# Kernel tuning notes

Hardware: AMD Instinct MI355X
Metric: run time of the kernel (lower is better)

The kernel has to match this reference:

```python
import jax, jax.numpy as jnp
import numpy as np
from jax import lax

STRIDES = (8, 16, 32, 64, 128)
LEVEL_HW = ((100, 128), (50, 64), (25, 32), (13, 16), (7, 8))
N, C = 16, 80
IMG_H, IMG_W = 800, 1024
THRESH = 0.05
IOU_THR = 0.6
PRE_NMS_K = 1000
POST_K = 100
CLS_OFFSET = 4096.0  # > max image coord, separates classes for batched NMS


def setup_inputs() -> dict:
    key = jax.random.key(0)
    ks = jax.random.split(key, 15)
    inp = {}
    for l, (h, w) in enumerate(LEVEL_HW):
        inp[f"cls{l}"] = jax.random.normal(ks[3 * l], (N, C, h, w), dtype=jnp.float32)
        # ltrb distances scaled to realistic pixel extents
        inp[f"reg{l}"] = jax.random.uniform(ks[3 * l + 1], (N, 4, h, w), dtype=jnp.float32) * 128.0
        inp[f"ctr{l}"] = jax.random.normal(ks[3 * l + 2], (N, 1, h, w), dtype=jnp.float32)
    return inp


def _level(cls, reg, ctr, stride):
    n, c, h, w = cls.shape
    sx = jnp.arange(w, dtype=jnp.float32) * stride + stride / 2.0
    sy = jnp.arange(h, dtype=jnp.float32) * stride + stride / 2.0
    px = jnp.broadcast_to(sx[None, :], (h, w)).reshape(-1)  # [hw]
    py = jnp.broadcast_to(sy[:, None], (h, w)).reshape(-1)  # [hw]
    # sqrt(cls_prob * centerness_prob), as in the source
    scores = jnp.sqrt(jax.nn.sigmoid(cls) * jax.nn.sigmoid(ctr))  # [n,c,h,w]
    scores = scores.transpose(0, 2, 3, 1).reshape(n, h * w, c)
    regf = reg.transpose(0, 2, 3, 1).reshape(n, h * w, 4)
    vals = scores.max(axis=-1)          # best class score per location
    labels = scores.argmax(axis=-1)
    vals = jnp.where(vals > THRESH, vals, 0.0)  # score threshold (zeroed instead of dropped)
    x1 = jnp.clip(px[None, :] - regf[..., 0], 0.0, IMG_W)
    y1 = jnp.clip(py[None, :] - regf[..., 1], 0.0, IMG_H)
    x2 = jnp.clip(px[None, :] + regf[..., 2], 0.0, IMG_W)
    y2 = jnp.clip(py[None, :] + regf[..., 3], 0.0, IMG_H)
    boxes = jnp.stack([x1, y1, x2, y2], axis=-1)  # [n,hw,4]
    return vals, labels, boxes


def _pairwise_iou(b):  # b: [K,4]
    area = (b[:, 2] - b[:, 0]) * (b[:, 3] - b[:, 1])
    lt = jnp.maximum(b[:, None, :2], b[None, :, :2])
    rb = jnp.minimum(b[:, None, 2:], b[None, :, 2:])
    wh = jnp.clip(rb - lt, 0.0)
    inter = wh[..., 0] * wh[..., 1]
    return inter / (area[:, None] + area[None, :] - inter + 1e-9)


def _nms_single(boxes, scores, labels):
    # class-aware NMS via per-class coordinate offset (torchvision batched_nms trick)
    ob = boxes + (labels.astype(boxes.dtype) * CLS_OFFSET)[:, None]
    iou = _pairwise_iou(ob)  # [K,K]
    K = boxes.shape[0]
    idxs = jnp.arange(K)

    def body(valid, i):
        keep_i = valid[i]
        valid = valid & ~(keep_i & (iou[i] > IOU_THR) & (idxs > i))
        return valid, keep_i

    _, keeps = lax.scan(body, scores > 0.0, idxs)  # greedy, scores already sorted desc
    kept_scores = jnp.where(keeps, scores, 0.0)
    top_vals, top = lax.top_k(kept_scores, POST_K)
    return boxes[top], top_vals, labels[top]


def _forward(levels):
    vals_l, labels_l, boxes_l = [], [], []
    for cls, reg, ctr, stride in levels:
        v, la, b = _level(cls, reg, ctr, stride)
        vals_l.append(v)
        labels_l.append(la)
        boxes_l.append(b)
    scores = jnp.concatenate(vals_l, axis=1)   # [N,P]
    labels = jnp.concatenate(labels_l, axis=1)  # [N,P]
    boxes = jnp.concatenate(boxes_l, axis=1)    # [N,P,4]
    tv, ti = lax.top_k(scores, PRE_NMS_K)       # pre-NMS top-k, sorted desc
    boxes_k = jnp.take_along_axis(boxes, ti[:, :, None], axis=1)
    labels_k = jnp.take_along_axis(labels, ti, axis=1)
    return jax.vmap(_nms_single)(boxes_k, tv, labels_k)


def reference(cls0, reg0, ctr0, cls1, reg1, ctr1, cls2, reg2, ctr2,
              cls3, reg3, ctr3, cls4, reg4, ctr4):
    levels = [
        (cls0, reg0, ctr0, 8), (cls1, reg1, ctr1, 16), (cls2, reg2, ctr2, 32),
        (cls3, reg3, ctr3, 64), (cls4, reg4, ctr4, 128),
    ]
    boxes, scores, labels = _forward(levels)
    return boxes, scores, labels  # [N,100,4], [N,100], [N,100]
```

## Files before the change

kernel.cpp:

```cpp
#include <hip/hip_runtime.h>
#include <stdint.h>

#pragma clang fp contract(off)

#define NB 16
#define NC 80
#define P_TOT 17064
#define P4 (P_TOT / 4)
#define PRE_K 1000
#define POST_K 100

__device__ __forceinline__ float sigmoidf_(float x) {
  return 1.0f / (1.0f + expf(-x));
}

__global__ __launch_bounds__(256, 2) void decode_kernel(
    const float* __restrict__ cls0, const float* __restrict__ reg0, const float* __restrict__ ctr0,
    const float* __restrict__ cls1, const float* __restrict__ reg1, const float* __restrict__ ctr1,
    const float* __restrict__ cls2, const float* __restrict__ reg2, const float* __restrict__ ctr2,
    const float* __restrict__ cls3, const float* __restrict__ reg3, const float* __restrict__ ctr3,
    const float* __restrict__ cls4, const float* __restrict__ reg4, const float* __restrict__ ctr4,
    int* __restrict__ labels, float* __restrict__ boxes,
    unsigned long long* __restrict__ keys)
{
  int quad = blockIdx.x * 64 + (threadIdx.x >> 2);
  int t4 = threadIdx.x & 3;
  int n = blockIdx.y;
  if (quad >= P4) return;
  int p0 = quad * 4;
  int off, wsh, hw; float stride; const float *cls, *reg, *ctr;
  if (p0 < 12800)      { off = 0;     wsh = 7; hw = 12800; stride = 8.f;   cls = cls0; reg = reg0; ctr = ctr0; }
  else if (p0 < 16000) { off = 12800; wsh = 6; hw = 3200;  stride = 16.f;  cls = cls1; reg = reg1; ctr = ctr1; }
  else if (p0 < 16800) { off = 16000; wsh = 5; hw = 800;   stride = 32.f;  cls = cls2; reg = reg2; ctr = ctr2; }
  else if (p0 < 17008) { off = 16800; wsh = 4; hw = 208;   stride = 64.f;  cls = cls3; reg = reg3; ctr = ctr3; }
  else                 { off = 17008; wsh = 3; hw = 56;    stride = 128.f; cls = cls4; reg = reg4; ctr = ctr4; }
  int loc0 = p0 - off;
  int y = loc0 >> wsh;
  int x0 = loc0 & ((1 << wsh) - 1);
  float py = (float)y * stride + 0.5f * stride;

  int c0 = t4 * 20;
  const float* cptr = cls + (size_t)n * NC * hw + (size_t)c0 * hw + loc0;
  float4 cv[20];
  #pragma unroll
  for (int k = 0; k < 20; ++k)
    cv[k] = *reinterpret_cast<const float4*>(cptr + (size_t)k * hw);

  float best[4] = { -3.4e38f, -3.4e38f, -3.4e38f, -3.4e38f };
  int bl[4] = { c0, c0, c0, c0 };
  #pragma unroll
  for (int k = 0; k < 20; ++k) {
    int c = c0 + k;
    if (cv[k].x > best[0]) { best[0] = cv[k].x; bl[0] = c; }
    if (cv[k].y > best[1]) { best[1] = cv[k].y; bl[1] = c; }
    if (cv[k].z > best[2]) { best[2] = cv[k].z; bl[2] = c; }
    if (cv[k].w > best[3]) { best[3] = cv[k].w; bl[3] = c; }
  }
  #pragma unroll
  for (int e = 0; e < 4; ++e) {
    #pragma unroll
    for (int d = 1; d <= 2; d <<= 1) {
      float ob = __shfl_xor(best[e], d);
      int ol = __shfl_xor(bl[e], d);
      if (ob > best[e] || (ob == best[e] && ol < bl[e])) { best[e] = ob; bl[e] = ol; }
    }
  }

  int e = t4;
  int loce = loc0 + e;
  float sctr_e = sigmoidf_(ctr[(size_t)n * hw + loce]);
  const float* rbase = reg + (size_t)n * 4 * hw + loce;
  float dl = rbase[0];
  float dt = rbase[(size_t)hw];
  float dr = rbase[(size_t)2 * hw];
  float db = rbase[(size_t)3 * hw];

  float s = sqrtf(sigmoidf_(best[e]) * sctr_e);
  float val = (s > 0.05f) ? s : 0.0f;
  float px = (float)(x0 + e) * stride + 0.5f * stride;
  float x1 = fminf(fmaxf(px - dl, 0.f), 1024.f);
  float y1 = fminf(fmaxf(py - dt, 0.f), 800.f);
  float x2 = fminf(fmaxf(px + dr, 0.f), 1024.f);
  float y2 = fminf(fmaxf(py + db, 0.f), 800.f);

  size_t o = (size_t)n * P_TOT + p0 + e;
  labels[o] = bl[e];
  *reinterpret_cast<float4*>(boxes + 4 * o) = make_float4(x1, y1, x2, y2);
  keys[o] = ((unsigned long long)__float_as_uint(val) << 32)
          | (unsigned long long)(0xFFFFFFFFu - (unsigned)(p0 + e));
}

__global__ __launch_bounds__(1024) void topgather_kernel(
    const unsigned long long* __restrict__ keys,
    const float* __restrict__ boxes, const int* __restrict__ labels,
    float* __restrict__ tboxes, float* __restrict__ tscores, int* __restrict__ tlabels)
{
  int n = blockIdx.x;
  int tid = threadIdx.x;
  int wave = tid >> 6;
  int lane = tid & 63;
  __shared__ unsigned hist[16384];
  __shared__ unsigned Wt[16], Wsuf[16];
  __shared__ unsigned s_d, s_M;
  __shared__ unsigned long long skey[2048];

  for (int i = tid; i < 16384; i += 1024) hist[i] = 0;
  __syncthreads();
  const unsigned long long* bk = keys + (size_t)n * P_TOT;
  for (int p = tid; p < P_TOT; p += 1024) {
    unsigned h = (unsigned)(bk[p] >> 48);
    atomicAdd(&hist[h], 1u);
  }
  __syncthreads();

  unsigned bvs[16];
  unsigned ssum = 0;
  #pragma unroll
  for (int q = 0; q < 16; ++q) { bvs[q] = hist[tid * 16 + q]; ssum += bvs[q]; }
  unsigned v = ssum;
  #pragma unroll
  for (int d = 1; d < 64; d <<= 1) {
    unsigned t = __shfl_down(v, d);
    if (lane + d < 64) v += t;
  }
  if (lane == 0) Wt[wave] = v;
  __syncthreads();
  if (wave == 0 && lane < 16) {
    unsigned wv = Wt[lane];
    unsigned own = wv;
    #pragma unroll
    for (int d = 1; d < 16; d <<= 1) {
      unsigned t = __shfl_down(wv, d);
      if (lane + d < 16) wv += t;
    }
    Wsuf[lane] = wv - own;
  }
  __syncthreads();
  unsigned At = v + Wsuf[wave];
  unsigned An = At - ssum;
  {
    if (At >= PRE_K && An < PRE_K) {
      unsigned cum = An;
      int d = tid * 16;
      unsigned M = 0;
      bool done = false;
      #pragma unroll
      for (int b = 15; b >= 0; --b) {
        if (!done) {
          cum += bvs[b];
          if (cum >= PRE_K) { d = tid * 16 + b; M = cum; done = true; }
        }
      }
      s_d = (unsigned)d;
      s_M = M;
    }
  }
  __syncthreads();
  unsigned dsel = s_d;
  {
    unsigned cum = An;
    #pragma unroll
    for (int b = 15; b >= 0; --b) {
      unsigned h = (unsigned)(tid * 16 + b);
      if (h >= dsel) hist[h] = cum << 16;
      cum += bvs[b];
    }
  }
  __syncthreads();
  for (int p = tid; p < P_TOT; p += 1024) {
    unsigned long long k = bk[p];
    unsigned h = (unsigned)(k >> 48);
    if (h >= dsel) {
      unsigned old = atomicAdd(&hist[h], 1u);
      unsigned slot = (old >> 16) + (old & 0xFFFFu);
      if (slot < 2048) skey[slot] = k;
    }
  }
  __syncthreads();
  unsigned Mcap = s_M < 2048u ? s_M : 2048u;
  #pragma unroll
  for (int e = 0; e < 2; ++e) {
    unsigned sidx = (unsigned)tid + e * 1024;
    if (sidx < Mcap) {
      unsigned long long k = skey[sidx];
      unsigned h = (unsigned)(k >> 48);
      unsigned info = hist[h];
      unsigned start = info >> 16;
      unsigned end = start + (info & 0xFFFFu);
      if (end > 2048u) end = 2048u;
      unsigned rank = 0;
      for (unsigned q = start; q < end; ++q)
        rank += (skey[q] > k) ? 1u : 0u;
      unsigned pos = start + rank;
      if (pos < PRE_K) {
        unsigned idx = 0xFFFFFFFFu - (unsigned)(k & 0xFFFFFFFFu);
        float sc = __uint_as_float((unsigned)(k >> 32));
        size_t src = (size_t)n * P_TOT + idx;
        size_t dst = (size_t)n * PRE_K + pos;
        tscores[dst] = sc;
        tlabels[dst] = labels[src];
        *reinterpret_cast<float4*>(tboxes + 4 * dst) =
            *reinterpret_cast<const float4*>(boxes + 4 * src);
      }
    }
  }
}

__global__ __launch_bounds__(128) void iou_kernel(
    const float* __restrict__ tboxes, const int* __restrict__ tlabels,
    unsigned long long* __restrict__ colsupp)
{
  int jb = blockIdx.x, w = blockIdx.y, n = blockIdx.z;
  int tid = threadIdx.x;
  int j = jb * 128 + tid;
  bool jvalid = (j < PRE_K);
  int ibase = w * 64;

  if (ibase >= jb * 128 + 128) {
    if (jvalid) colsupp[((size_t)n * PRE_K + j) * 16 + w] = 0ULL;
    return;
  }

  __shared__ float4 sb[64];
  __shared__ float sa[64];
  if (tid < 64) {
    int i = ibase + tid;
    float4 v = make_float4(0.f, 0.f, 0.f, 0.f);
    if (i < PRE_K) {
      const float* b = tboxes + ((size_t)n * PRE_K + i) * 4;
      float offv = (float)tlabels[(size_t)n * PRE_K + i] * 4096.0f;
      v = make_float4(b[0] + offv, b[1] + offv, b[2] + offv, b[3] + offv);
    }
    sb[tid] = v;
    sa[tid] = (v.z - v.x) * (v.w - v.y);
  }
  __syncthreads();

  float4 bj = make_float4(0.f, 0.f, 0.f, 0.f);
  if (jvalid) {
    const float* b = tboxes + ((size_t)n * PRE_K + j) * 4;
    float offv = (float)tlabels[(size_t)n * PRE_K + j] * 4096.0f;
    bj = make_float4(b[0] + offv, b[1] + offv, b[2] + offv, b[3] + offv);
  }
  float aj = (bj.z - bj.x) * (bj.w - bj.y);

  unsigned long long m = 0, mb = 0;
  #pragma unroll
  for (int b = 0; b < 64; ++b) {
    float4 bi = sb[b];
    float ai = sa[b];
    float lx = fmaxf(bi.x, bj.x), ly = fmaxf(bi.y, bj.y);
    float rx = fminf(bi.z, bj.z), ry = fminf(bi.w, bj.w);
    float iw = fmaxf(rx - lx, 0.f), ih = fmaxf(ry - ly, 0.f);
    float inter = iw * ih;
    float denom = ai + aj - inter + 1e-9f;
    float t = inter - 0.6f * denom;
    if (t > 0.f) m |= (1ull << b);
    if (fabsf(t) <= denom * 7.62939453125e-6f) mb |= (1ull << b);
  }
  if (mb) {
    unsigned long long r = mb;
    while (r) {
      int b = __ffsll(r) - 1; r &= r - 1;
      float4 bi = sb[b];
      float ai = sa[b];
      float lx = fmaxf(bi.x, bj.x), ly = fmaxf(bi.y, bj.y);
      float rx = fminf(bi.z, bj.z), ry = fminf(bi.w, bj.w);
      float iw = fmaxf(rx - lx, 0.f), ih = fmaxf(ry - ly, 0.f);
      float inter = iw * ih;
      float denom = ai + aj - inter + 1e-9f;
      float iou = inter / denom;
      if (iou > 0.6f) m |= (1ull << b); else m &= ~(1ull << b);
    }
  }
  unsigned long long tri;
  if (ibase >= j) tri = 0ULL;
  else if (j - ibase >= 64) tri = ~0ULL;
  else tri = (1ull << (j - ibase)) - 1ull;
  m &= tri;
  if (jvalid) colsupp[((size_t)n * PRE_K + j) * 16 + w] = m;
}

__global__ __launch_bounds__(1024) void greedyfin_kernel(
    const unsigned long long* __restrict__ colsupp, const float* __restrict__ tscores,
    const float* __restrict__ tboxes, const int* __restrict__ tlabels,
    float* __restrict__ out)
{
  int n = blockIdx.x;
  int tid = threadIdx.x;
  int wave = tid >> 6;
  int lane = tid & 63;
  __shared__ unsigned long long T[136 * 64];
  __shared__ unsigned long long keptw[16];

  {
    int wq = wave;
    int j = wq * 64 + lane;
    int base = (wq * (wq + 1)) / 2;
    if (j < PRE_K) {
      const unsigned long long* C = colsupp + ((size_t)n * PRE_K + j) * 16;
      for (int c = 0; c <= wq; ++c) T[(base + c) * 64 + lane] = C[c];
    } else {
      for (int c = 0; c <= wq; ++c) T[(base + c) * 64 + lane] = 0ULL;
    }
  }
  __syncthreads();

  if (wave == 0) {
    const float* sc = tscores + (size_t)n * PRE_K;
    float sval[16];
    #pragma unroll
    for (int k = 0; k < 16; ++k) {
      int j = k * 64 + lane;
      sval[k] = (j < PRE_K) ? sc[j] : 0.f;
    }
    unsigned removedbits = 0;
    #pragma unroll
    for (int c = 0; c < 16; ++c) {
      unsigned long long col = T[((c * (c + 1)) / 2 + c) * 64 + lane];
      unsigned long long sp = __ballot(sval[c] > 0.f);
      unsigned long long inc = __ballot(((removedbits >> c) & 1u) != 0u);
      unsigned long long K = sp & ~inc;
      unsigned long long kept = 0;
      for (int it = 0; it < 64; ++it) {
        unsigned long long Bsupp = __ballot((col & K) != 0ULL);
        unsigned long long Snew = K & ~Bsupp & ~kept;
        if (Snew == 0ULL) break;
        kept |= Snew;
        unsigned long long Bd = __ballot((col & kept) != 0ULL);
        K &= ~Bd;
      }
      if ((col & kept) != 0ULL) removedbits |= (1u << c);
      #pragma unroll
      for (int w = 0; w < 16; ++w) {
        if (w > c) {
          unsigned long long xw = T[((w * (w + 1)) / 2 + c) * 64 + lane];
          if ((xw & kept) != 0ULL) removedbits |= (1u << w);
        }
      }
      if (lane == 0) keptw[c] = kept;
    }
  }
  __syncthreads();

  __shared__ unsigned sk[1024];
  __shared__ unsigned sz[1024];
  bool inr = (tid < PRE_K);
  bool keep = inr && (((keptw[tid >> 6] >> (tid & 63)) & 1ull) != 0ull);
  sk[tid] = keep ? 1u : 0u;
  sz[tid] = (inr && !keep) ? 1u : 0u;
  __syncthreads();
  for (int ofs = 1; ofs < 1024; ofs <<= 1) {
    unsigned a = (tid >= ofs) ? sk[tid - ofs] : 0;
    unsigned b = (tid >= ofs) ? sz[tid - ofs] : 0;
    __syncthreads();
    sk[tid] += a; sz[tid] += b;
    __syncthreads();
  }
  int nk = (int)sk[1023];
  int slot = -1;
  if (inr) {
    if (keep) {
      int r = (int)sk[tid] - 1;
      if (r < POST_K) slot = r;
    } else {
      int r = nk + (int)sz[tid] - 1;
      if (r < POST_K) slot = r;
    }
  }
  if (slot >= 0) {
    size_t src = (size_t)n * PRE_K + tid;
    size_t ob = ((size_t)n * POST_K + slot) * 4;
    out[ob+0] = tboxes[4*src+0];
    out[ob+1] = tboxes[4*src+1];
    out[ob+2] = tboxes[4*src+2];
    out[ob+3] = tboxes[4*src+3];
    out[(size_t)NB*POST_K*4 + (size_t)n*POST_K + slot] = keep ? tscores[src] : 0.0f;
    out[(size_t)NB*POST_K*5 + (size_t)n*POST_K + slot] = (float)tlabels[src];
  }
}

extern "C" void kernel_launch(void* const* d_in, const int* in_sizes, int n_in,
                              void* d_out, int out_size, void* d_ws, size_t ws_size,
                              hipStream_t stream) {
  char* w = (char*)d_ws;
  auto carve = [&](size_t bytes) { char* p = w; w += (bytes + 255) & ~(size_t)255; return p; };
  int* labels   = (int*)carve((size_t)NB * P_TOT * 4);
  float* boxes  = (float*)carve((size_t)NB * P_TOT * 16);
  unsigned long long* keys = (unsigned long long*)carve((size_t)NB * P_TOT * 8);
  unsigned long long* colsupp = (unsigned long long*)carve((size_t)NB * PRE_K * 16 * 8);
  float* tboxes  = (float*)carve((size_t)NB * PRE_K * 16);
  float* tscores = (float*)carve((size_t)NB * PRE_K * 4);
  int* tlabels   = (int*)carve((size_t)NB * PRE_K * 4);

  const float* cls0 = (const float*)d_in[0];
  const float* reg0 = (const float*)d_in[1];
  const float* ctr0 = (const float*)d_in[2];
  const float* cls1 = (const float*)d_in[3];
  const float* reg1 = (const float*)d_in[4];
  const float* ctr1 = (const float*)d_in[5];
  const float* cls2 = (const float*)d_in[6];
  const float* reg2 = (const float*)d_in[7];
  const float* ctr2 = (const float*)d_in[8];
  const float* cls3 = (const float*)d_in[9];
  const float* reg3 = (const float*)d_in[10];
  const float* ctr3 = (const float*)d_in[11];
  const float* cls4 = (const float*)d_in[12];
  const float* reg4 = (const float*)d_in[13];
  const float* ctr4 = (const float*)d_in[14];

  dim3 dg((P4 + 63) / 64, NB);
  decode_kernel<<<dg, 256, 0, stream>>>(cls0, reg0, ctr0, cls1, reg1, ctr1,
                                        cls2, reg2, ctr2, cls3, reg3, ctr3,
                                        cls4, reg4, ctr4,
                                        labels, boxes, keys);
  topgather_kernel<<<NB, 1024, 0, stream>>>(keys, boxes, labels,
                                            tboxes, tscores, tlabels);
  dim3 gi(8, 16, NB);
  iou_kernel<<<gi, 128, 0, stream>>>(tboxes, tlabels, colsupp);
  greedyfin_kernel<<<NB, 1024, 0, stream>>>(colsupp, tscores, tboxes, tlabels, (float*)d_out);
}
```

Measured before the change: 67.42 us.

## Fuse top-k gather, IoU mask, and greedy NMS into one per-image kernel

Merges the top-k selection, pairwise IoU suppression-mask computation and greedy NMS/finalize kernels into a single tail kernel with one block per image. Selected boxes, scores, labels and the triangular mask stay in LDS, aliased over the histogram buffer, so the global round trips and two launches go away. The cost is that IoU work moves from 2048 small blocks spread across the GPU to 16 blocks of 1024 threads, which cuts parallelism and raises LDS use per block.

```diff
diff --git a/kernel.cpp b/kernel.cpp
--- a/kernel.cpp
+++ b/kernel.cpp
@@ -90,22 +90,38 @@
           | (unsigned long long)(0xFFFFFFFFu - (unsigned)(p0 + e));
 }
 
-__global__ __launch_bounds__(1024) void topgather_kernel(
+__global__ __launch_bounds__(1024) void tail_kernel(
     const unsigned long long* __restrict__ keys,
     const float* __restrict__ boxes, const int* __restrict__ labels,
-    float* __restrict__ tboxes, float* __restrict__ tscores, int* __restrict__ tlabels)
+    float* __restrict__ out)
 {
   int n = blockIdx.x;
   int tid = threadIdx.x;
   int wave = tid >> 6;
   int lane = tid & 63;
-  __shared__ unsigned hist[16384];
+
+  __shared__ __align__(16) char smem0[16384 * 4 + 2048 * 8];
+  unsigned* hist = (unsigned*)smem0;
+  unsigned long long* skey = (unsigned long long*)(smem0 + 16384 * 4);
+  unsigned long long* T = (unsigned long long*)smem0;
+  __shared__ float4 tbo[1024];
+  __shared__ float areas[1024];
+  __shared__ float4 tb[1024];
+  __shared__ float sc[1024];
+  __shared__ int lb[1024];
   __shared__ unsigned Wt[16], Wsuf[16];
   __shared__ unsigned s_d, s_M;
-  __shared__ unsigned long long skey[2048];
+  __shared__ unsigned long long keptw[16];
+  __shared__ unsigned sk[1024], sz[1024];
 
   for (int i = tid; i < 16384; i += 1024) hist[i] = 0;
-  __syncthreads();
+  tbo[tid] = make_float4(0.f, 0.f, 0.f, 0.f);
+  areas[tid] = 0.f;
+  tb[tid] = make_float4(0.f, 0.f, 0.f, 0.f);
+  sc[tid] = 0.f;
+  lb[tid] = 0;
+  __syncthreads();
+
   const unsigned long long* bk = keys + (size_t)n * P_TOT;
   for (int p = tid; p < P_TOT; p += 1024) {
     unsigned h = (unsigned)(bk[p] >> 48);
@@ -138,22 +154,20 @@
   __syncthreads();
   unsigned At = v + Wsuf[wave];
   unsigned An = At - ssum;
-  {
-    if (At >= PRE_K && An < PRE_K) {
-      unsigned cum = An;
-      int d = tid * 16;
-      unsigned M = 0;
-      bool done = false;
-      #pragma unroll
-      for (int b = 15; b >= 0; --b) {
-        if (!done) {
-          cum += bvs[b];
-          if (cum >= PRE_K) { d = tid * 16 + b; M = cum; done = true; }
-        }
-      }
-      s_d = (unsigned)d;
-      s_M = M;
-    }
+  if (At >= PRE_K && An < PRE_K) {
+    unsigned cum = An;
+    int d = tid * 16;
+    unsigned M = 0;
+    bool done = false;
+    #pragma unroll
+    for (int b = 15; b >= 0; --b) {
+      if (!done) {
+        cum += bvs[b];
+        if (cum >= PRE_K) { d = tid * 16 + b; M = cum; done = true; }
+      }
+    }
+    s_d = (unsigned)d;
+    s_M = M;
   }
   __syncthreads();
   unsigned dsel = s_d;
@@ -194,126 +208,69 @@
       unsigned pos = start + rank;
       if (pos < PRE_K) {
         unsigned idx = 0xFFFFFFFFu - (unsigned)(k & 0xFFFFFFFFu);
-        float sc = __uint_as_float((unsigned)(k >> 32));
+        float scv = __uint_as_float((unsigned)(k >> 32));
         size_t src = (size_t)n * P_TOT + idx;
-        size_t dst = (size_t)n * PRE_K + pos;
-        tscores[dst] = sc;
-        tlabels[dst] = labels[src];
-        *reinterpret_cast<float4*>(tboxes + 4 * dst) =
-            *reinterpret_cast<const float4*>(boxes + 4 * src);
-      }
-    }
-  }
-}
-
-__global__ __launch_bounds__(128) void iou_kernel(
-    const float* __restrict__ tboxes, const int* __restrict__ tlabels,
-    unsigned long long* __restrict__ colsupp)
-{
-  int jb = blockIdx.x, w = blockIdx.y, n = blockIdx.z;
-  int tid = threadIdx.x;
-  int j = jb * 128 + tid;
-  bool jvalid = (j < PRE_K);
-  int ibase = w * 64;
-
-  if (ibase >= jb * 128 + 128) {
-    if (jvalid) colsupp[((size_t)n * PRE_K + j) * 16 + w] = 0ULL;
-    return;
-  }
-
-  __shared__ float4 sb[64];
-  __shared__ float sa[64];
-  if (tid < 64) {
-    int i = ibase + tid;
-    float4 v = make_float4(0.f, 0.f, 0.f, 0.f);
-    if (i < PRE_K) {
-      const float* b = tboxes + ((size_t)n * PRE_K + i) * 4;
-      float offv = (float)tlabels[(size_t)n * PRE_K + i] * 4096.0f;
-      v = make_float4(b[0] + offv, b[1] + offv, b[2] + offv, b[3] + offv);
-    }
-    sb[tid] = v;
-    sa[tid] = (v.z - v.x) * (v.w - v.y);
-  }
-  __syncthreads();
-
-  float4 bj = make_float4(0.f, 0.f, 0.f, 0.f);
-  if (jvalid) {
-    const float* b = tboxes + ((size_t)n * PRE_K + j) * 4;
-    float offv = (float)tlabels[(size_t)n * PRE_K + j] * 4096.0f;
-    bj = make_float4(b[0] + offv, b[1] + offv, b[2] + offv, b[3] + offv);
-  }
-  float aj = (bj.z - bj.x) * (bj.w - bj.y);
-
-  unsigned long long m = 0, mb = 0;
-  #pragma unroll
-  for (int b = 0; b < 64; ++b) {
-    float4 bi = sb[b];
-    float ai = sa[b];
-    float lx = fmaxf(bi.x, bj.x), ly = fmaxf(bi.y, bj.y);
-    float rx = fminf(bi.z, bj.z), ry = fminf(bi.w, bj.w);
-    float iw = fmaxf(rx - lx, 0.f), ih = fmaxf(ry - ly, 0.f);
-    float inter = iw * ih;
-    float denom = ai + aj - inter + 1e-9f;
-    float t = inter - 0.6f * denom;
-    if (t > 0.f) m |= (1ull << b);
-    if (fabsf(t) <= denom * 7.62939453125e-6f) mb |= (1ull << b);
-  }
-  if (mb) {
-    unsigned long long r = mb;
-    while (r) {
-      int b = __ffsll(r) - 1; r &= r - 1;
-      float4 bi = sb[b];
-      float ai = sa[b];
+        float4 b4 = *reinterpret_cast<const float4*>(boxes + 4 * src);
+        int L = labels[src];
+        float offv = (float)L * 4096.0f;
+        float4 bo = make_float4(b4.x + offv, b4.y + offv, b4.z + offv, b4.w + offv);
+        tb[pos] = b4;
+        sc[pos] = scv;
+        lb[pos] = L;
+        tbo[pos] = bo;
+        areas[pos] = (bo.z - bo.x) * (bo.w - bo.y);
+      }
+    }
+  }
+  __syncthreads();
+
+  for (int p = wave; p < 136; p += 16) {
+    int w = 0;
+    while ((w + 1) * (w + 2) / 2 <= p) ++w;
+    int c = p - w * (w + 1) / 2;
+    int j = w * 64 + lane;
+    float4 bj = tbo[j];
+    float aj = areas[j];
+    unsigned long long m = 0, mb = 0;
+    int ibase = c * 64;
+    #pragma unroll
+    for (int b = 0; b < 64; ++b) {
+      float4 bi = tbo[ibase + b];
+      float ai = areas[ibase + b];
       float lx = fmaxf(bi.x, bj.x), ly = fmaxf(bi.y, bj.y);
       float rx = fminf(bi.z, bj.z), ry = fminf(bi.w, bj.w);
       float iw = fmaxf(rx - lx, 0.f), ih = fmaxf(ry - ly, 0.f);
       float inter = iw * ih;
       float denom = ai + aj - inter + 1e-9f;
-      float iou = inter / denom;
-      if (iou > 0.6f) m |= (1ull << b); else m &= ~(1ull << b);
-    }
-  }
-  unsigned long long tri;
-  if (ibase >= j) tri = 0ULL;
-  else if (j - ibase >= 64) tri = ~0ULL;
-  else tri = (1ull << (j - ibase)) - 1ull;
-  m &= tri;
-  if (jvalid) colsupp[((size_t)n * PRE_K + j) * 16 + w] = m;
-}
-
-__global__ __launch_bounds__(1024) void greedyfin_kernel(
-    const unsigned long long* __restrict__ colsupp, const float* __restrict__ tscores,
-    const float* __restrict__ tboxes, const int* __restrict__ tlabels,
-    float* __restrict__ out)
-{
-  int n = blockIdx.x;
-  int tid = threadIdx.x;
-  int wave = tid >> 6;
-  int lane = tid & 63;
-  __shared__ unsigned long long T[136 * 64];
-  __shared__ unsigned long long keptw[16];
-
-  {
-    int wq = wave;
-    int j = wq * 64 + lane;
-    int base = (wq * (wq + 1)) / 2;
-    if (j < PRE_K) {
-      const unsigned long long* C = colsupp + ((size_t)n * PRE_K + j) * 16;
-      for (int c = 0; c <= wq; ++c) T[(base + c) * 64 + lane] = C[c];
-    } else {
-      for (int c = 0; c <= wq; ++c) T[(base + c) * 64 + lane] = 0ULL;
-    }
+      float t = inter - 0.6f * denom;
+      if (t > 0.f) m |= (1ull << b);
+      if (fabsf(t) <= denom * 7.62939453125e-6f) mb |= (1ull << b);
+    }
+    if (mb) {
+      unsigned long long r = mb;
+      while (r) {
+        int b = __ffsll(r) - 1; r &= r - 1;
+        float4 bi = tbo[ibase + b];
+        float ai = areas[ibase + b];
+        float lx = fmaxf(bi.x, bj.x), ly = fmaxf(bi.y, bj.y);
+        float rx = fminf(bi.z, bj.z), ry = fminf(bi.w, bj.w);
+        float iw = fmaxf(rx - lx, 0.f), ih = fmaxf(ry - ly, 0.f);
+        float inter = iw * ih;
+        float denom = ai + aj - inter + 1e-9f;
+        float iou = inter / denom;
+        if (iou > 0.6f) m |= (1ull << b); else m &= ~(1ull << b);
+      }
+    }
+    if (j >= PRE_K) m = 0ULL;
+    else if (c == w) m &= (1ull << lane) - 1ull;
+    T[(size_t)p * 64 + lane] = m;
   }
   __syncthreads();
 
   if (wave == 0) {
-    const float* sc = tscores + (size_t)n * PRE_K;
     float sval[16];
     #pragma unroll
-    for (int k = 0; k < 16; ++k) {
-      int j = k * 64 + lane;
-      sval[k] = (j < PRE_K) ? sc[j] : 0.f;
-    }
+    for (int k = 0; k < 16; ++k) sval[k] = sc[k * 64 + lane];
     unsigned removedbits = 0;
     #pragma unroll
     for (int c = 0; c < 16; ++c) {
@@ -343,8 +300,6 @@
   }
   __syncthreads();
 
-  __shared__ unsigned sk[1024];
-  __shared__ unsigned sz[1024];
   bool inr = (tid < PRE_K);
   bool keep = inr && (((keptw[tid >> 6] >> (tid & 63)) & 1ull) != 0ull);
   sk[tid] = keep ? 1u : 0u;
@@ -369,14 +324,11 @@
     }
   }
   if (slot >= 0) {
-    size_t src = (size_t)n * PRE_K + tid;
     size_t ob = ((size_t)n * POST_K + slot) * 4;
-    out[ob+0] = tboxes[4*src+0];
-    out[ob+1] = tboxes[4*src+1];
-    out[ob+2] = tboxes[4*src+2];
-    out[ob+3] = tboxes[4*src+3];
-    out[(size_t)NB*POST_K*4 + (size_t)n*POST_K + slot] = keep ? tscores[src] : 0.0f;
-    out[(size_t)NB*POST_K*5 + (size_t)n*POST_K + slot] = (float)tlabels[src];
+    float4 b4 = tb[tid];
+    out[ob+0] = b4.x; out[ob+1] = b4.y; out[ob+2] = b4.z; out[ob+3] = b4.w;
+    out[(size_t)NB*POST_K*4 + (size_t)n*POST_K + slot] = keep ? sc[tid] : 0.0f;
+    out[(size_t)NB*POST_K*5 + (size_t)n*POST_K + slot] = (float)lb[tid];
   }
 }
 
@@ -388,10 +340,6 @@
   int* labels   = (int*)carve((size_t)NB * P_TOT * 4);
   float* boxes  = (float*)carve((size_t)NB * P_TOT * 16);
   unsigned long long* keys = (unsigned long long*)carve((size_t)NB * P_TOT * 8);
-  unsigned long long* colsupp = (unsigned long long*)carve((size_t)NB * PRE_K * 16 * 8);
-  float* tboxes  = (float*)carve((size_t)NB * PRE_K * 16);
-  float* tscores = (float*)carve((size_t)NB * PRE_K * 4);
-  int* tlabels   = (int*)carve((size_t)NB * PRE_K * 4);
 
   const float* cls0 = (const float*)d_in[0];
   const float* reg0 = (const float*)d_in[1];
@@ -414,9 +362,5 @@
                                         cls2, reg2, ctr2, cls3, reg3, ctr3,
                                         cls4, reg4, ctr4,
                                         labels, boxes, keys);
-  topgather_kernel<<<NB, 1024, 0, stream>>>(keys, boxes, labels,
-                                            tboxes, tscores, tlabels);
-  dim3 gi(8, 16, NB);
-  iou_kernel<<<gi, 128, 0, stream>>>(tboxes, tlabels, colsupp);
-  greedyfin_kernel<<<NB, 1024, 0, stream>>>(colsupp, tscores, tboxes, tlabels, (float*)d_out);
+  tail_kernel<<<NB, 1024, 0, stream>>>(keys, boxes, labels, (float*)d_out);
 }
```

Result: slower. 130.1 us (+93.0%).
